# Optimization experiments

Measured on AMD Instinct MI355X. Metric: run time of the kernel, lower is better.

Reference implementation:

```python
import jax, jax.numpy as jnp
import numpy as np

B, S, H, HK, D = 2, 2048, 32, 8, 128
R = 128            # rotary_dim
SINK = 128         # sink_len (always-visible prefix tokens in KV cache)
MAXPOS = 4096
BASE = 10000.0
SCALE = 0.08838834764831845  # 1/sqrt(head_size)
NEG = -1e30


def setup_inputs() -> dict:
    key = jax.random.key(0)
    ks = jax.random.split(key, 5)
    q = jax.random.normal(ks[0], (B, S, H, D), jnp.float32)
    k = jax.random.normal(ks[1], (B, S, HK, D), jnp.float32)
    v = jax.random.normal(ks[2], (B, S, HK, D), jnp.float32)
    sink_k = jax.random.normal(ks[3], (B, SINK, HK, D), jnp.float32)
    sink_v = jax.random.normal(ks[4], (B, SINK, HK, D), jnp.float32)
    # vLLM-style cache: row p = concat(cos(p*inv_freq), sin(p*inv_freq)), each R/2 wide
    inv_freq = 1.0 / (BASE ** (jnp.arange(0, R, 2, dtype=jnp.float32) / R))
    t = jnp.arange(MAXPOS, dtype=jnp.float32)
    freqs = jnp.outer(t, inv_freq)                      # [MAXPOS, R/2]
    cos_sin_cache = jnp.concatenate([jnp.cos(freqs), jnp.sin(freqs)], axis=-1)
    positions = jnp.arange(S, dtype=jnp.int32)
    return {"q": q, "k": k, "v": v, "sink_k": sink_k, "sink_v": sink_v,
            "cos_sin_cache": cos_sin_cache, "positions": positions}


def _apply_rope_neox(x, cos, sin):
    # x: [B, S, N, D]; cos/sin: [S, R/2]
    x_rot, x_pass = x[..., :R], x[..., R:]
    half = R // 2
    x1, x2 = x_rot[..., :half], x_rot[..., half:]
    c = cos[None, :, None, :]
    s = sin[None, :, None, :]
    o1 = x1 * c - x2 * s
    o2 = x2 * c + x1 * s
    return jnp.concatenate([o1, o2, x_pass], axis=-1)


def reference(q, k, v, sink_k, sink_v, cos_sin_cache, positions):
    # RoPE on q and k (sink KV already cached post-RoPE at their positions)
    cos_sin = cos_sin_cache[positions]                  # [S, R]
    cos, sin = cos_sin[:, :R // 2], cos_sin[:, R // 2:]
    q = _apply_rope_neox(q, cos, sin)
    k = _apply_rope_neox(k, cos, sin)

    # Prepend sink KV: effective kv length = SINK + S
    k_full = jnp.concatenate([sink_k, k], axis=1)       # [B, SINK+S, HK, D]
    v_full = jnp.concatenate([sink_v, v], axis=1)

    # GQA: expand kv heads to query heads
    rep = H // HK
    k_full = jnp.repeat(k_full, rep, axis=2)            # [B, SINK+S, H, D]
    v_full = jnp.repeat(v_full, rep, axis=2)

    scores = jnp.einsum('bqhd,bkhd->bhqk', q, k_full) * SCALE  # [B,H,S,SINK+S]

    # sink tokens always visible; causal over the real sequence
    q_idx = jnp.arange(S)[:, None]
    k_idx = jnp.arange(SINK + S)[None, :]
    mask = (k_idx < SINK) | ((k_idx - SINK) <= q_idx)   # [S, SINK+S]
    scores = jnp.where(mask[None, None], scores, NEG)

    attn = jax.nn.softmax(scores, axis=-1)
    out = jnp.einsum('bhqk,bkhd->bqhd', attn, v_full)   # [B,S,H,D]
    return out
```

## Files before the change

kernel.cpp:

```cpp
#include <hip/hip_runtime.h>

#define B_    2
#define S_    2048
#define H_    32
#define HK_   8
#define D_    128
#define SINK_ 128
#define KV_   (SINK_ + S_)
#define SCALE_L2E 0.12752139f

typedef unsigned short u16;
typedef unsigned int   u32;
typedef float  f32x4  __attribute__((ext_vector_type(4)));
typedef __bf16 bf16x8 __attribute__((ext_vector_type(8)));
typedef short  s16x8  __attribute__((ext_vector_type(8)));

__device__ __forceinline__ u16 f2bf(float f) {
    union { float f; u32 u; } c; c.f = f;
    u32 u = c.u;
    return (u16)((u + 0x7FFFu + ((u >> 16) & 1u)) >> 16);
}
__device__ __forceinline__ float bf2f(u16 u) {
    union { u32 u; float f; } c; c.u = ((u32)u) << 16; return c.f;
}

#define PREPK_BLOCKS 8704
#define PREPV_BLOCKS 544

__global__ __launch_bounds__(256) void prep_kv(
    const float* __restrict__ k, const float* __restrict__ sk,
    const float* __restrict__ v, const float* __restrict__ sv,
    const float* __restrict__ csc, const int* __restrict__ pos,
    u16* __restrict__ kall,
    u16* __restrict__ vt)
{
    __shared__ u16 t[128][66];
    const int tid = threadIdx.x;
    if ((int)blockIdx.x < PREPK_BLOCKS) {
        int g  = blockIdx.x * 256 + tid;
        int i  = g & 63;
        int rw = g >> 6;
        int bh = rw / KV_;
        int j  = rw - bh * KV_;
        int hk = bh & (HK_ - 1);
        int b  = bh >> 3;
        float o1, o2;
        if (j < SINK_) {
            size_t src = ((size_t)(b * SINK_ + j) * HK_ + hk) * D_;
            o1 = sk[src + i]; o2 = sk[src + 64 + i];
        } else {
            int sq = j - SINK_;
            size_t src = ((size_t)(b * S_ + sq) * HK_ + hk) * D_;
            float x1 = k[src + i];
            float x2 = k[src + 64 + i];
            int p = pos[sq];
            float c = csc[p * D_ + i], sn = csc[p * D_ + 64 + i];
            o1 = x1 * c - x2 * sn;
            o2 = x2 * c + x1 * sn;
        }
        kall[(size_t)rw * D_ + i]      = f2bf(o1);
        kall[(size_t)rw * D_ + 64 + i] = f2bf(o2);
    } else {
        int blk = blockIdx.x - PREPK_BLOCKS;
        int bh = blk / 34;
        int jt = (blk - bh * 34) * 64;
        int hk = bh & (HK_ - 1), b = bh >> 3;
        int d1 = tid & 127;
        int j0 = tid >> 7;
        #pragma unroll
        for (int p = 0; p < 32; ++p) {
            int jl = j0 + 2 * p;
            int j  = jt + jl;
            float x;
            if (j < SINK_) x = sv[((size_t)(b * SINK_ + j) * HK_ + hk) * D_ + d1];
            else           x = v[((size_t)(b * S_ + (j - SINK_)) * HK_ + hk) * D_ + d1];
            t[d1][jl] = f2bf(x);
        }
        __syncthreads();
        int d0 = tid >> 5;
        int jl = (tid & 31) * 2;
        #pragma unroll
        for (int p = 0; p < 16; ++p) {
            int dd = d0 + 8 * p;
            u32 pk = (u32)t[dd][jl] | ((u32)t[dd][jl + 1] << 16);
            *(u32*)(vt + ((size_t)bh * D_ + dd) * KV_ + jt + jl) = pk;
        }
    }
}

__global__ __launch_bounds__(256, 3) void flash_kernel(
    const float* __restrict__ q,
    const float* __restrict__ csc,
    const int*   __restrict__ pos,
    const u16*   __restrict__ kall,
    const u16*   __restrict__ vt,
    float* __restrict__ out)
{
    __shared__ u16 lk[64][136];
    __shared__ u16 lv[128][72];
    __shared__ u16 lp[4][16][72];

    const int tid  = threadIdx.x;
    const int lane = tid & 63, w = tid >> 6;
    const int col  = lane & 15, grp = lane >> 4;
    const int rowb = grp * 4;

    const int hk = blockIdx.x & 7;
    int tdec = blockIdx.x >> 3;
    const int b  = tdec & 1; tdec >>= 1;
    const int hr = tdec & 3; tdec >>= 2;
    const int ts = 31 - tdec;
    const int h  = hk * 4 + hr;
    const int s0 = ts * 64;
    const int nfull = 2 + ts;

    const int srow = s0 + w * 16 + col;
    const float* qg = q + ((size_t)(b * S_ + srow) * H_ + h) * D_;
    const float* cp = csc + (size_t)pos[srow] * D_;
    bf16x8 qf[4];
    {
        float xa[4][8], cs0[8], cs1[8], sn0[8], sn1[8];
        #pragma unroll
        for (int c = 0; c < 4; ++c) {
            *(float4*)&xa[c][0] = *(const float4*)(qg + c * 32 + grp * 8);
            *(float4*)&xa[c][4] = *(const float4*)(qg + c * 32 + grp * 8 + 4);
        }
        *(float4*)&cs0[0] = *(const float4*)(cp + grp * 8);
        *(float4*)&cs0[4] = *(const float4*)(cp + grp * 8 + 4);
        *(float4*)&cs1[0] = *(const float4*)(cp + 32 + grp * 8);
        *(float4*)&cs1[4] = *(const float4*)(cp + 32 + grp * 8 + 4);
        *(float4*)&sn0[0] = *(const float4*)(cp + 64 + grp * 8);
        *(float4*)&sn0[4] = *(const float4*)(cp + 64 + grp * 8 + 4);
        *(float4*)&sn1[0] = *(const float4*)(cp + 96 + grp * 8);
        *(float4*)&sn1[4] = *(const float4*)(cp + 96 + grp * 8 + 4);
        #pragma unroll
        for (int j = 0; j < 8; ++j) {
            qf[0][j] = (__bf16)((xa[0][j] * cs0[j] - xa[2][j] * sn0[j]) * SCALE_L2E);
            qf[1][j] = (__bf16)((xa[1][j] * cs1[j] - xa[3][j] * sn1[j]) * SCALE_L2E);
            qf[2][j] = (__bf16)((xa[2][j] * cs0[j] + xa[0][j] * sn0[j]) * SCALE_L2E);
            qf[3][j] = (__bf16)((xa[3][j] * cs1[j] + xa[1][j] * sn1[j]) * SCALE_L2E);
        }
    }

    const u16* kb = kall + (size_t)(b * HK_ + hk) * KV_ * D_;
    const u16* vb = vt   + (size_t)(b * HK_ + hk) * D_ * KV_;

    f32x4 of[8];
    #pragma unroll
    for (int nt = 0; nt < 8; ++nt) of[nt] = (f32x4){0.f, 0.f, 0.f, 0.f};
    float rs[4] = {0.f, 0.f, 0.f, 0.f};

    s16x8 kr[4], vr[4];
    {
        const u16* gk = kb;
        #pragma unroll
        for (int i = 0; i < 4; ++i) {
            int g = tid + i * 256;
            kr[i] = *(const s16x8*)(gk + g * 8);
            vr[i] = *(const s16x8*)(vb + (size_t)(g >> 3) * KV_ + (g & 7) * 8);
        }
    }

    for (int it = 0; it <= nfull; ++it) {
        __syncthreads();
        #pragma unroll
        for (int i = 0; i < 4; ++i) {
            int g = tid + i * 256;
            *(s16x8*)(&lk[g >> 4][(g & 15) * 8]) = kr[i];
            *(s16x8*)(&lv[g >> 3][(g & 7) * 8]) = vr[i];
        }
        if (it < nfull) {
            const int kt = (it + 1) * 64;
            const u16* gk = kb + (size_t)kt * D_;
            #pragma unroll
            for (int i = 0; i < 4; ++i) {
                int g = tid + i * 256;
                kr[i] = *(const s16x8*)(gk + g * 8);
                vr[i] = *(const s16x8*)(vb + (size_t)(g >> 3) * KV_ + kt + (g & 7) * 8);
            }
        }
        __syncthreads();

        f32x4 sv4[4];
        #pragma unroll
        for (int ct = 0; ct < 4; ++ct) {
            f32x4 acc = (f32x4){0.f, 0.f, 0.f, 0.f};
            #pragma unroll
            for (int c = 0; c < 4; ++c) {
                bf16x8 bf = __builtin_bit_cast(bf16x8,
                    *(const s16x8*)(&lk[ct * 16 + col][c * 32 + grp * 8]));
                acc = __builtin_amdgcn_mfma_f32_16x16x32_bf16(qf[c], bf, acc, 0, 0, 0);
            }
            sv4[ct] = acc;
        }

        if (it == nfull) {
            #pragma unroll
            for (int ct = 0; ct < 4; ++ct)
                #pragma unroll
                for (int r = 0; r < 4; ++r)
                    if (ct * 16 + col > w * 16 + rowb + r) sv4[ct][r] = -1e30f;
        }

        #pragma unroll
        for (int ct = 0; ct < 4; ++ct) {
            #pragma unroll
            for (int r = 0; r < 4; ++r) {
                float p = __builtin_amdgcn_exp2f(sv4[ct][r]);
                u16 pb = f2bf(p);
                rs[r] += bf2f(pb);
                lp[w][rowb + r][((ct ^ grp) << 4) + col] = pb;
            }
        }

        asm volatile("s_waitcnt lgkmcnt(0)" ::: "memory");

        #pragma unroll
        for (int kc = 0; kc < 2; ++kc) {
            const int cgrp = (((kc << 1) | (grp >> 1)) ^ (col >> 2));
            bf16x8 ap = __builtin_bit_cast(bf16x8,
                *(const s16x8*)(&lp[w][col][(cgrp << 4) + ((grp & 1) << 3)]));
            #pragma unroll
            for (int nt = 0; nt < 8; ++nt) {
                bf16x8 bv = __builtin_bit_cast(bf16x8,
                    *(const s16x8*)(&lv[nt * 16 + col][kc * 32 + grp * 8]));
                of[nt] = __builtin_amdgcn_mfma_f32_16x16x32_bf16(ap, bv, of[nt], 0, 0, 0);
            }
        }
    }

    float rc[4];
    #pragma unroll
    for (int r = 0; r < 4; ++r) {
        float t = rs[r];
        t += __shfl_xor(t, 1);
        t += __shfl_xor(t, 2);
        t += __shfl_xor(t, 4);
        t += __shfl_xor(t, 8);
        rc[r] = 1.0f / t;
    }
    #pragma unroll
    for (int nt = 0; nt < 8; ++nt) {
        #pragma unroll
        for (int r = 0; r < 4; ++r) {
            int sr = s0 + w * 16 + rowb + r;
            out[((size_t)(b * S_ + sr) * H_ + h) * D_ + nt * 16 + col] = of[nt][r] * rc[r];
        }
    }
}

__global__ __launch_bounds__(256) void sink_attn_scalar(
    const float* __restrict__ q, const float* __restrict__ k,
    const float* __restrict__ v, const float* __restrict__ sink_k,
    const float* __restrict__ sink_v, const float* __restrict__ cs_cache,
    const int* __restrict__ positions, float* __restrict__ out)
{
    const int wave = threadIdx.x >> 6;
    const int lane = threadIdx.x & 63;
    const int half = lane >> 5;
    const int l = lane & 31;
    const int d0 = 2 * l;
    const int g = blockIdx.x * 4 + wave;
    const int s = g & (S_ - 1);
    const int bh = g >> 11;
    const int h = bh & (H_ - 1);
    const int b = bh >> 5;
    const int hk = h >> 2;
    const float* cs = cs_cache + positions[s] * D_;
    float2 cq = *(const float2*)(cs + d0);
    float2 sq = *(const float2*)(cs + 64 + d0);
    const float* qrow = q + (size_t)((b * S_ + s) * H_ + h) * D_;
    float2 qa = *(const float2*)(qrow + d0);
    float2 qb = *(const float2*)(qrow + 64 + d0);
    const float q0 = (qa.x * cq.x - qb.x * sq.x) * SCALE_L2E;
    const float q1 = (qa.y * cq.y - qb.y * sq.y) * SCALE_L2E;
    const float q2 = (qb.x * cq.x + qa.x * sq.x) * SCALE_L2E;
    const float q3 = (qb.y * cq.y + qa.y * sq.y) * SCALE_L2E;
    float m = -1e30f, L = 0.0f;
    float a0 = 0.f, a1 = 0.f, a2 = 0.f, a3 = 0.f;
    const int nk = SINK_ + s + 1;
    for (int jj = 0; jj < nk; jj += 2) {
        const int j = jj + half;
        const bool valid = (j < nk);
        const int je = valid ? j : (nk - 1);
        const float* vrow;
        float k0, k1, k2, k3;
        if (je < SINK_) {
            const int off = ((b * SINK_ + je) * HK_ + hk) * D_;
            vrow = sink_v + off;
            float2 ka = *(const float2*)(sink_k + off + d0);
            float2 kb = *(const float2*)(sink_k + off + 64 + d0);
            k0 = ka.x; k1 = ka.y; k2 = kb.x; k3 = kb.y;
        } else {
            const int sk = je - SINK_;
            const int off = ((b * S_ + sk) * HK_ + hk) * D_;
            vrow = v + off;
            float2 ka = *(const float2*)(k + off + d0);
            float2 kb = *(const float2*)(k + off + 64 + d0);
            const float* csk = cs_cache + positions[sk] * D_;
            float2 cc = *(const float2*)(csk + d0);
            float2 ss = *(const float2*)(csk + 64 + d0);
            k0 = ka.x * cc.x - kb.x * ss.x;
            k1 = ka.y * cc.y - kb.y * ss.y;
            k2 = kb.x * cc.x + ka.x * ss.x;
            k3 = kb.y * cc.y + ka.y * ss.y;
        }
        float p = q0 * k0 + q1 * k1 + q2 * k2 + q3 * k3;
        p += __shfl_xor(p, 16); p += __shfl_xor(p, 8);
        p += __shfl_xor(p, 4);  p += __shfl_xor(p, 2); p += __shfl_xor(p, 1);
        if (!valid) p = -1e30f;
        const float mn = fmaxf(m, p);
        const float corr = __builtin_amdgcn_exp2f(m - mn);
        const float pe = __builtin_amdgcn_exp2f(p - mn);
        float2 va = *(const float2*)(vrow + d0);
        float2 vb = *(const float2*)(vrow + 64 + d0);
        L = L * corr + pe;
        a0 = a0 * corr + pe * va.x; a1 = a1 * corr + pe * va.y;
        a2 = a2 * corr + pe * vb.x; a3 = a3 * corr + pe * vb.y;
        m = mn;
    }
    const float mo = __shfl_xor(m, 32);
    const float Lo = __shfl_xor(L, 32);
    const float b0f = __shfl_xor(a0, 32);
    const float b1f = __shfl_xor(a1, 32);
    const float b2f = __shfl_xor(a2, 32);
    const float b3f = __shfl_xor(a3, 32);
    const float M = fmaxf(m, mo);
    const float c_s = __builtin_amdgcn_exp2f(m - M);
    const float c_o = __builtin_amdgcn_exp2f(mo - M);
    const float r = 1.0f / (L * c_s + Lo * c_o);
    float* orow = out + (size_t)((b * S_ + s) * H_ + h) * D_;
    float2 o2v;
    if (half == 0) { o2v.x = (a0 * c_s + b0f * c_o) * r; o2v.y = (a1 * c_s + b1f * c_o) * r; }
    else           { o2v.x = (a2 * c_s + b2f * c_o) * r; o2v.y = (a3 * c_s + b3f * c_o) * r; }
    *(float2*)(orow + half * 64 + d0) = o2v;
}

extern "C" void kernel_launch(void* const* d_in, const int* in_sizes, int n_in,
                              void* d_out, int out_size, void* d_ws, size_t ws_size,
                              hipStream_t stream) {
    const float* q      = (const float*)d_in[0];
    const float* k      = (const float*)d_in[1];
    const float* v      = (const float*)d_in[2];
    const float* sink_k = (const float*)d_in[3];
    const float* sink_v = (const float*)d_in[4];
    const float* cs     = (const float*)d_in[5];
    const int*   pos    = (const int*)d_in[6];
    float* out          = (float*)d_out;

    const size_t kall_elems = (size_t)B_ * HK_ * KV_ * D_;
    const size_t need = 2 * kall_elems * sizeof(u16);

    if (ws_size < need) {
        const int rows = B_ * H_ * S_;
        sink_attn_scalar<<<dim3(rows / 4), dim3(256), 0, stream>>>(
            q, k, v, sink_k, sink_v, cs, pos, out);
        return;
    }

    u16* kall = (u16*)d_ws;
    u16* vtp  = kall + kall_elems;

    prep_kv<<<dim3(PREPK_BLOCKS + PREPV_BLOCKS), dim3(256), 0, stream>>>(
        k, sink_k, v, sink_v, cs, pos, kall, vtp);
    flash_kernel<<<dim3(2048), dim3(256), 0, stream>>>(q, cs, pos, kall, vtp, out);
}
```

Baseline: 287.9 us.

## Compute S transposed to keep P in registers, dropping LDS round trip

The QK^T MFMA now has its operands swapped so the score tile comes out transposed (keys along the register dimension). K rows are permuted as they are stored to LDS, so each lane's accumulator values line up directly with the A-operand layout of the PV MFMA. This removes the LDS staging buffer for P, its write/read and the waitcnt, and shrinks the row-sum to one register with a cross-lane reduction at the end. Freeing LDS and registers also allows raising the occupancy hint to 4 blocks per CU, at the cost of a more intricate index permutation and causal-mask mapping that must be exactly right.

Measured after the change: 283.5 us. No clear change (-1.5%).

```diff
diff --git a/kernel.cpp b/kernel.cpp
--- a/kernel.cpp
+++ b/kernel.cpp
@@ -19,9 +19,6 @@
     union { float f; u32 u; } c; c.f = f;
     u32 u = c.u;
     return (u16)((u + 0x7FFFu + ((u >> 16) & 1u)) >> 16);
-}
-__device__ __forceinline__ float bf2f(u16 u) {
-    union { u32 u; float f; } c; c.u = ((u32)u) << 16; return c.f;
 }
 
 #define PREPK_BLOCKS 8704
@@ -88,7 +85,7 @@
     }
 }
 
-__global__ __launch_bounds__(256, 3) void flash_kernel(
+__global__ __launch_bounds__(256, 4) void flash_kernel(
     const float* __restrict__ q,
     const float* __restrict__ csc,
     const int*   __restrict__ pos,
@@ -98,7 +95,6 @@
 {
     __shared__ u16 lk[64][136];
     __shared__ u16 lv[128][72];
-    __shared__ u16 lp[4][16][72];
 
     const int tid  = threadIdx.x;
     const int lane = tid & 63, w = tid >> 6;
@@ -148,7 +144,7 @@
     f32x4 of[8];
     #pragma unroll
     for (int nt = 0; nt < 8; ++nt) of[nt] = (f32x4){0.f, 0.f, 0.f, 0.f};
-    float rs[4] = {0.f, 0.f, 0.f, 0.f};
+    float rs = 0.f;
 
     s16x8 kr[4], vr[4];
     {
@@ -166,7 +162,9 @@
         #pragma unroll
         for (int i = 0; i < 4; ++i) {
             int g = tid + i * 256;
-            *(s16x8*)(&lk[g >> 4][(g & 15) * 8]) = kr[i];
+            int j = g >> 4;
+            int pj = (j & 0x23) | ((j & 4) << 2) | ((j & 0x18) >> 1);
+            *(s16x8*)(&lk[pj][(g & 15) * 8]) = kr[i];
             *(s16x8*)(&lv[g >> 3][(g & 7) * 8]) = vr[i];
         }
         if (it < nfull) {
@@ -187,58 +185,57 @@
             f32x4 acc = (f32x4){0.f, 0.f, 0.f, 0.f};
             #pragma unroll
             for (int c = 0; c < 4; ++c) {
-                bf16x8 bf = __builtin_bit_cast(bf16x8,
+                bf16x8 kf = __builtin_bit_cast(bf16x8,
                     *(const s16x8*)(&lk[ct * 16 + col][c * 32 + grp * 8]));
-                acc = __builtin_amdgcn_mfma_f32_16x16x32_bf16(qf[c], bf, acc, 0, 0, 0);
+                acc = __builtin_amdgcn_mfma_f32_16x16x32_bf16(kf, qf[c], acc, 0, 0, 0);
             }
             sv4[ct] = acc;
         }
 
         if (it == nfull) {
             #pragma unroll
-            for (int ct = 0; ct < 4; ++ct)
+            for (int ct = 0; ct < 4; ++ct) {
+                const int keybase = (ct >> 1) * 32 + (ct & 1) * 4 + grp * 8;
                 #pragma unroll
                 for (int r = 0; r < 4; ++r)
-                    if (ct * 16 + col > w * 16 + rowb + r) sv4[ct][r] = -1e30f;
-        }
-
-        #pragma unroll
-        for (int ct = 0; ct < 4; ++ct) {
-            #pragma unroll
-            for (int r = 0; r < 4; ++r) {
-                float p = __builtin_amdgcn_exp2f(sv4[ct][r]);
-                u16 pb = f2bf(p);
-                rs[r] += bf2f(pb);
-                lp[w][rowb + r][((ct ^ grp) << 4) + col] = pb;
-            }
-        }
-
-        asm volatile("s_waitcnt lgkmcnt(0)" ::: "memory");
-
+                    if (keybase + r > w * 16 + col) sv4[ct][r] = -1e30f;
+            }
+        }
+
+        bf16x8 ap[2];
         #pragma unroll
         for (int kc = 0; kc < 2; ++kc) {
-            const int cgrp = (((kc << 1) | (grp >> 1)) ^ (col >> 2));
-            bf16x8 ap = __builtin_bit_cast(bf16x8,
-                *(const s16x8*)(&lp[w][col][(cgrp << 4) + ((grp & 1) << 3)]));
+            #pragma unroll
+            for (int h2 = 0; h2 < 2; ++h2) {
+                const int ct = kc * 2 + h2;
+                #pragma unroll
+                for (int r = 0; r < 4; ++r) {
+                    float p = __builtin_amdgcn_exp2f(sv4[ct][r]);
+                    __bf16 pb = (__bf16)p;
+                    rs += (float)pb;
+                    ap[kc][h2 * 4 + r] = pb;
+                }
+            }
+        }
+
+        #pragma unroll
+        for (int kc = 0; kc < 2; ++kc) {
             #pragma unroll
             for (int nt = 0; nt < 8; ++nt) {
                 bf16x8 bv = __builtin_bit_cast(bf16x8,
                     *(const s16x8*)(&lv[nt * 16 + col][kc * 32 + grp * 8]));
-                of[nt] = __builtin_amdgcn_mfma_f32_16x16x32_bf16(ap, bv, of[nt], 0, 0, 0);
-            }
-        }
-    }
-
+                of[nt] = __builtin_amdgcn_mfma_f32_16x16x32_bf16(ap[kc], bv, of[nt], 0, 0, 0);
+            }
+        }
+    }
+
+    rs += __shfl_xor(rs, 16);
+    rs += __shfl_xor(rs, 32);
     float rc[4];
     #pragma unroll
-    for (int r = 0; r < 4; ++r) {
-        float t = rs[r];
-        t += __shfl_xor(t, 1);
-        t += __shfl_xor(t, 2);
-        t += __shfl_xor(t, 4);
-        t += __shfl_xor(t, 8);
-        rc[r] = 1.0f / t;
-    }
+    for (int r = 0; r < 4; ++r)
+        rc[r] = 1.0f / __shfl(rs, grp * 4 + r);
+
     #pragma unroll
     for (int nt = 0; nt < 8; ++nt) {
         #pragma unroll
```
